# Performance work log

Hardware: AMD Instinct MI355X
Metric: run time of the kernel (lower is better)

The kernel has to match this reference:

```python
import jax, jax.numpy as jnp
import numpy as np
from jax import lax

KERNEL = (2, 2)
STRIDE = (1, 1)

def setup_inputs() -> dict:
    key = jax.random.key(0)
    x = jax.random.normal(key, (16, 96, 224, 224), dtype=jnp.float32)
    return {"x": x}

def reference(x):
    # Valid max pooling over NCHW with window KERNEL, stride STRIDE.
    kR, kC = KERNEL
    sR, sC = STRIDE
    return lax.reduce_window(
        x,
        -jnp.inf,
        lax.max,
        window_dimensions=(1, 1, kR, kC),
        window_strides=(1, 1, sR, sC),
        padding="VALID",
    )
```

## Files before the change

kernel.cpp:

```cpp
#include <hip/hip_runtime.h>


#define W_IN   224
#define HW_IN  (224 * 224)
#define W_OUT  223
#define H_OUT  223

typedef float f4a __attribute__((ext_vector_type(4)));
typedef float f4u __attribute__((ext_vector_type(4), aligned(4)));

__global__ __launch_bounds__(256) void maxpool2x2_s1_v4_kernel(
    const float* __restrict__ in, float* __restrict__ out, int total4) {
  int t = blockIdx.x * 256 + threadIdx.x;
  if (t >= total4) return;

  int base = t * 4;
  int w  = base % W_OUT;
  int r  = base / W_OUT;

  if (w <= W_OUT - 4) {
    int h  = r % H_OUT;
    int nc = r / H_OUT;
    const float* p = in + (size_t)nc * HW_IN + h * W_IN + w;
    f4u a = *(const f4u*)p;
    float a4 = p[4];
    f4u b = *(const f4u*)(p + W_IN);
    float b4 = p[W_IN + 4];

    f4a o;
    o.x = fmaxf(fmaxf(a.x, a.y), fmaxf(b.x, b.y));
    o.y = fmaxf(fmaxf(a.y, a.z), fmaxf(b.y, b.z));
    o.z = fmaxf(fmaxf(a.z, a.w), fmaxf(b.z, b.w));
    o.w = fmaxf(fmaxf(a.w, a4),  fmaxf(b.w, b4));
    *(f4a*)(out + base) = o;
  } else {
    f4a o;
    #pragma unroll
    for (int j = 0; j < 4; ++j) {
      int idx = base + j;
      int wj  = idx % W_OUT;
      int tj  = idx / W_OUT;
      int hj  = tj % H_OUT;
      int ncj = tj / H_OUT;
      const float* p = in + (size_t)ncj * HW_IN + hj * W_IN + wj;
      float m0 = fmaxf(p[0], p[1]);
      float m1 = fmaxf(p[W_IN], p[W_IN + 1]);
      ((float*)&o)[j] = fmaxf(m0, m1);
    }
    *(f4a*)(out + base) = o;
  }
}

extern "C" void kernel_launch(void* const* d_in, const int* in_sizes, int n_in,
                              void* d_out, int out_size, void* d_ws, size_t ws_size,
                              hipStream_t stream) {
  const float* x = (const float*)d_in[0];
  float* out = (float*)d_out;
  const int total = 16 * 96 * H_OUT * W_OUT;
  const int total4 = total / 4;
  const int blocks = (total4 + 255) / 256;
  maxpool2x2_s1_v4_kernel<<<blocks, 256, 0, stream>>>(x, out, total4);
}
```

Baseline: 531.9 us.

## Process 8-row vertical strips per thread to reuse input rows

Each thread now walks 8 output rows down a 4-column group, carrying the previous input row in registers so each input row is loaded once instead of twice. Input loads become aligned 16-byte vector loads, and the per-element index division is replaced by a single decomposition per thread. The cost is less parallelism, since there are 8x fewer threads, and output stores that are no longer 16-byte aligned because of the odd 223-wide output row.

```diff
diff --git a/kernel.cpp b/kernel.cpp
--- a/kernel.cpp
+++ b/kernel.cpp
@@ -1,53 +1,64 @@
 #include <hip/hip_runtime.h>
 
 
-#define W_IN   224
-#define HW_IN  (224 * 224)
-#define W_OUT  223
-#define H_OUT  223
+#define W_IN    224
+#define HW_IN   (224 * 224)
+#define W_OUT   223
+#define H_OUT   223
+#define HW_OUT  (223 * 223)
+#define CGROUPS 56
+#define RSTRIPS 28
 
 typedef float f4a __attribute__((ext_vector_type(4)));
 typedef float f4u __attribute__((ext_vector_type(4), aligned(4)));
 
-__global__ __launch_bounds__(256) void maxpool2x2_s1_v4_kernel(
-    const float* __restrict__ in, float* __restrict__ out, int total4) {
-  int t = blockIdx.x * 256 + threadIdx.x;
-  if (t >= total4) return;
+__global__ __launch_bounds__(256) void maxpool2x2_s1_strip8(
+    const float* __restrict__ in, float* __restrict__ out) {
+  int job = blockIdx.x * 256 + threadIdx.x;
+  int cg  = job % CGROUPS;
+  int t   = job / CGROUPS;
+  int rs  = t % RSTRIPS;
+  int nc  = t / RSTRIPS;
 
-  int base = t * 4;
-  int w  = base % W_OUT;
-  int r  = base / W_OUT;
+  int w  = cg * 4;
+  int h0 = rs * 8;
+  int nrows   = (rs == RSTRIPS - 1) ? 7 : 8;
+  bool tailc  = (cg == CGROUPS - 1);
 
-  if (w <= W_OUT - 4) {
-    int h  = r % H_OUT;
-    int nc = r / H_OUT;
-    const float* p = in + (size_t)nc * HW_IN + h * W_IN + w;
-    f4u a = *(const f4u*)p;
-    float a4 = p[4];
-    f4u b = *(const f4u*)(p + W_IN);
-    float b4 = p[W_IN + 4];
+  const float* p = in  + (size_t)nc * HW_IN  + (size_t)h0 * W_IN  + w;
+  float*       q = out + (size_t)nc * HW_OUT + (size_t)h0 * W_OUT + w;
 
-    f4a o;
-    o.x = fmaxf(fmaxf(a.x, a.y), fmaxf(b.x, b.y));
-    o.y = fmaxf(fmaxf(a.y, a.z), fmaxf(b.y, b.z));
-    o.z = fmaxf(fmaxf(a.z, a.w), fmaxf(b.z, b.w));
-    o.w = fmaxf(fmaxf(a.w, a4),  fmaxf(b.w, b4));
-    *(f4a*)(out + base) = o;
-  } else {
-    f4a o;
-    #pragma unroll
-    for (int j = 0; j < 4; ++j) {
-      int idx = base + j;
-      int wj  = idx % W_OUT;
-      int tj  = idx / W_OUT;
-      int hj  = tj % H_OUT;
-      int ncj = tj / H_OUT;
-      const float* p = in + (size_t)ncj * HW_IN + hj * W_IN + wj;
-      float m0 = fmaxf(p[0], p[1]);
-      float m1 = fmaxf(p[W_IN], p[W_IN + 1]);
-      ((float*)&o)[j] = fmaxf(m0, m1);
+  f4a a = *(const f4a*)p;
+  float a4 = tailc ? a.w : p[4];
+
+  #pragma unroll 4
+  for (int r = 0; r < nrows; ++r) {
+    p += W_IN;
+    f4a b = *(const f4a*)p;
+    float b4 = tailc ? b.w : p[4];
+
+    float vx = fmaxf(a.x, b.x);
+    float vy = fmaxf(a.y, b.y);
+    float vz = fmaxf(a.z, b.z);
+    float vw = fmaxf(a.w, b.w);
+    float v4 = fmaxf(a4, b4);
+
+    if (!tailc) {
+      f4u o;
+      o.x = fmaxf(vx, vy);
+      o.y = fmaxf(vy, vz);
+      o.z = fmaxf(vz, vw);
+      o.w = fmaxf(vw, v4);
+      *(f4u*)q = o;
+    } else {
+      q[0] = fmaxf(vx, vy);
+      q[1] = fmaxf(vy, vz);
+      q[2] = fmaxf(vz, vw);
     }
-    *(f4a*)(out + base) = o;
+    q += W_OUT;
+
+    a = b;
+    a4 = b4;
   }
 }
 
@@ -56,8 +67,7 @@
                               hipStream_t stream) {
   const float* x = (const float*)d_in[0];
   float* out = (float*)d_out;
-  const int total = 16 * 96 * H_OUT * W_OUT;
-  const int total4 = total / 4;
-  const int blocks = (total4 + 255) / 256;
-  maxpool2x2_s1_v4_kernel<<<blocks, 256, 0, stream>>>(x, out, total4);
+  const int jobs   = 16 * 96 * RSTRIPS * CGROUPS;
+  const int blocks = jobs / 256;
+  maxpool2x2_s1_strip8<<<blocks, 256, 0, stream>>>(x, out);
 }
```

Measured after the change: 523.9 us. No clear change (-1.5%).
